# Kernel optimization log

Hardware: AMD Instinct MI355X
Metric: run time of the kernel (lower is better)

The kernel has to match this reference:

```python
import jax, jax.numpy as jnp
import numpy as np

INPUT_DIM, HIDDEN_DIM, OUTPUT_DIM = 64, 256, 32
BATCH, SEQ = 256, 1024
# AutoNCP(256, 32, sparsity_level=0.5): motor=32, command=max(int(0.4*224),1)=89, inter=135
LAYER_HID = [135, 89, 32]
LAYER_IN = [INPUT_DIM, 135, 89]


def setup_inputs() -> dict:
    key = jax.random.key(0)
    ks = iter(jax.random.split(key, 64))
    d = {}
    d["x"] = jax.random.normal(next(ks), (BATCH, SEQ, INPUT_DIM), dtype=jnp.float32)
    for l, (fin, hid) in enumerate(zip(LAYER_IN, LAYER_HID)):
        sp = jax.random.bernoulli(next(ks), 0.5, (hid, fin))
        d[f"mask{l}"] = jnp.concatenate([sp, jnp.ones((hid, hid), dtype=bool)], axis=1)
        scale = 1.0 / np.sqrt(fin + hid)
        for name in ("W1", "W2", "Wa", "Wb"):
            d[f"{name}_{l}"] = jax.random.normal(next(ks), (hid, fin + hid), dtype=jnp.float32) * scale
        for name in ("b1", "b2", "ba", "bb"):
            d[f"{name}_{l}"] = jnp.zeros((hid,), dtype=jnp.float32)
    d["fc_W"] = jax.random.normal(next(ks), (HIDDEN_DIM, HIDDEN_DIM), dtype=jnp.float32) * (1.0 / np.sqrt(HIDDEN_DIM))
    d["fc_b"] = jnp.zeros((HIDDEN_DIM,), dtype=jnp.float32)
    return d


def _cfc_cell(inp, h, mask, W1, b1, W2, b2, Wa, ba, Wb, bb):
    # ncps CfCCell, mode='default', no backbone, ts = 1.0
    x = jnp.concatenate([inp, h], axis=1)
    m = mask.astype(W1.dtype)
    ff1 = jnp.tanh(x @ (W1 * m).T + b1)
    ff2 = jnp.tanh(x @ (W2 * m).T + b2)
    t = jax.nn.sigmoid(x @ Wa.T + ba + x @ Wb.T + bb)  # sigmoid(t_a*ts + t_b), ts=1
    return ff1 * (1.0 - t) + t * ff2


def _forward(x, masks, layer_params, fc_W, fc_b):
    B = x.shape[0]
    init = tuple(jnp.zeros((B, h), dtype=x.dtype) for h in LAYER_HID)

    def step(carry, xt):
        hs = list(carry)
        inp = xt
        for l in range(3):  # inter -> command -> motor (WiredCfCCell)
            hs[l] = _cfc_cell(inp, hs[l], masks[l], *layer_params[l])
            inp = hs[l]
        return tuple(hs), None

    carry, _ = jax.lax.scan(step, init, jnp.swapaxes(x, 0, 1))  # scan over time [T,B,D]
    hn = jnp.concatenate(carry, axis=1)  # [B, HIDDEN_DIM] full state
    return hn @ fc_W.T + fc_b


def reference(x, mask0, mask1, mask2,
              W1_0, b1_0, W2_0, b2_0, Wa_0, ba_0, Wb_0, bb_0,
              W1_1, b1_1, W2_1, b2_1, Wa_1, ba_1, Wb_1, bb_1,
              W1_2, b1_2, W2_2, b2_2, Wa_2, ba_2, Wb_2, bb_2,
              fc_W, fc_b):
    masks = (mask0, mask1, mask2)
    lp = ((W1_0, b1_0, W2_0, b2_0, Wa_0, ba_0, Wb_0, bb_0),
          (W1_1, b1_1, W2_1, b2_1, Wa_1, ba_1, Wb_1, bb_1),
          (W1_2, b1_2, W2_2, b2_2, Wa_2, ba_2, Wb_2, bb_2))
    return _forward(x, masks, lp, fc_W, fc_b)
```

## Files before the change

### kernel.cpp

```cpp
#include <hip/hip_runtime.h>


typedef _Float16 half2v __attribute__((ext_vector_type(2)));
typedef _Float16 half8v __attribute__((ext_vector_type(8)));

#define NBLK   256
#define NTHR   512
#define TSTEPS 1024
#define KPAD   224
#define WSTRIDE 232
#define KHALF  112
#define NKB    14

struct Ptrs {
    const float* x;
    const unsigned int* msk[3];
    const float* W1[3];
    const float* W2[3];
    const float* Wa[3];
    const float* Wb[3];
    const float* b1[3];
    const float* b2[3];
    const float* ba[3];
    const float* bb[3];
    const float* fcW;
    const float* fcb;
};

__device__ __forceinline__ float fexp2(float x) {
#if __has_builtin(__builtin_amdgcn_exp2f)
    return __builtin_amdgcn_exp2f(x);
#else
    return exp2f(x);
#endif
}
__device__ __forceinline__ float frcp(float x) {
#if __has_builtin(__builtin_amdgcn_rcpf)
    return __builtin_amdgcn_rcpf(x);
#else
    return 1.0f / x;
#endif
}
__device__ __forceinline__ float fsig(float x) {
    return frcp(1.0f + fexp2(-1.442695041f * x));
}
__device__ __forceinline__ float ftanh(float x) {
    return 2.0f * frcp(1.0f + fexp2(-2.885390082f * x)) - 1.0f;
}

#if __has_builtin(__builtin_amdgcn_fdot2)
#define FD(a, b, c) __builtin_amdgcn_fdot2((a), (b), (c), false)
#else
__device__ __forceinline__ float fd_fallback(half2v a, half2v b, float c) {
    return c + (float)a[0] * (float)b[0] + (float)a[1] * (float)b[1];
}
#define FD(a, b, c) fd_fallback((a), (b), (c))
#endif

__device__ __forceinline__ half2v h2(_Float16 a, _Float16 b) { return half2v{a, b}; }

__device__ __forceinline__ half2v fold2(const float* Wp, const unsigned int* mkp,
                                        int nK, int K, int k0) {
    float u0 = 0.f, u1 = 0.f;
    if (k0 < K) {
        const int i0 = nK + k0;
        u0 = Wp[i0] * ((mkp[i0] != 0u) ? 1.0f : 0.0f);
    }
    if (k0 + 1 < K) {
        const int i1 = nK + k0 + 1;
        u1 = Wp[i1] * ((mkp[i1] != 0u) ? 1.0f : 0.0f);
    }
    return h2((_Float16)u0, (_Float16)u1);
}

#define DECL_KB(kb) \
    const half2v w1_##kb##_0 = fold2(W1p, mkp, nK, K, koff + kb * 8 + 0); \
    const half2v w1_##kb##_1 = fold2(W1p, mkp, nK, K, koff + kb * 8 + 2); \
    const half2v w1_##kb##_2 = fold2(W1p, mkp, nK, K, koff + kb * 8 + 4); \
    const half2v w1_##kb##_3 = fold2(W1p, mkp, nK, K, koff + kb * 8 + 6); \
    const half2v w2_##kb##_0 = fold2(W2p, mkp, nK, K, koff + kb * 8 + 0); \
    const half2v w2_##kb##_1 = fold2(W2p, mkp, nK, K, koff + kb * 8 + 2); \
    const half2v w2_##kb##_2 = fold2(W2p, mkp, nK, K, koff + kb * 8 + 4); \
    const half2v w2_##kb##_3 = fold2(W2p, mkp, nK, K, koff + kb * 8 + 6);

#define DOT_KB(kb) { \
    const half8v xv = *(const half8v*)(srcp + kb * 8); \
    const half8v wv = *(const half8v*)(wap + kb * 8); \
    ac00 = FD(h2(xv[0], xv[1]), w1_##kb##_0, ac00); \
    ac10 = FD(h2(xv[0], xv[1]), w2_##kb##_0, ac10); \
    ac20 = FD(h2(xv[0], xv[1]), h2(wv[0], wv[1]), ac20); \
    ac01 = FD(h2(xv[2], xv[3]), w1_##kb##_1, ac01); \
    ac11 = FD(h2(xv[2], xv[3]), w2_##kb##_1, ac11); \
    ac21 = FD(h2(xv[2], xv[3]), h2(wv[2], wv[3]), ac21); \
    ac00 = FD(h2(xv[4], xv[5]), w1_##kb##_2, ac00); \
    ac10 = FD(h2(xv[4], xv[5]), w2_##kb##_2, ac10); \
    ac20 = FD(h2(xv[4], xv[5]), h2(wv[4], wv[5]), ac20); \
    ac01 = FD(h2(xv[6], xv[7]), w1_##kb##_3, ac01); \
    ac11 = FD(h2(xv[6], xv[7]), w2_##kb##_3, ac11); \
    ac21 = FD(h2(xv[6], xv[7]), h2(wv[6], wv[7]), ac21); \
}

__global__ __launch_bounds__(NTHR, 2)
void cfc_kernel(Ptrs P, float* __restrict__ out) {
    __shared__ __align__(16) _Float16 xc[2][3][KPAD];
    __shared__ __align__(16) _Float16 waL[256][WSTRIDE];
    __shared__ __align__(16) float hn[256];

    const int tid  = threadIdx.x;
    const int b    = blockIdx.x;
    const int unit = tid >> 1;
    const int half = tid & 1;

    int L, n;
    if (unit < 135)      { L = 0; n = unit; }
    else if (unit < 224) { L = 1; n = unit - 135; }
    else                 { L = 2; n = unit - 224; }
    const int K    = (L == 0) ? 199 : ((L == 1) ? 224 : 121);
    const int HOFF = (L == 0) ? 0   : ((L == 1) ? 135 : 224);

    {
        int* z = (int*)&xc[0][0][0];
        for (int i = tid; i < 2 * 3 * KPAD / 2; i += NTHR) z[i] = 0;
    }

    const float* W1p        = P.W1[L];
    const float* W2p        = P.W2[L];
    const float* Wap        = P.Wa[L];
    const float* Wbp        = P.Wb[L];
    const unsigned int* mkp = P.msk[L];
    const int nK   = n * K;
    const int koff = half * KHALF;

    DECL_KB(0)  DECL_KB(1)  DECL_KB(2)  DECL_KB(3)  DECL_KB(4)
    DECL_KB(5)  DECL_KB(6)  DECL_KB(7)  DECL_KB(8)  DECL_KB(9)
    DECL_KB(10) DECL_KB(11) DECL_KB(12) DECL_KB(13)

#pragma unroll
    for (int i = 0; i < KHALF / 2; ++i) {
        const int k0 = koff + 2 * i;
        float a0 = 0.f, a1 = 0.f;
        if (k0 < K)     a0 = Wap[nK + k0] + Wbp[nK + k0];
        if (k0 + 1 < K) a1 = Wap[nK + k0 + 1] + Wbp[nK + k0 + 1];
        *(half2v*)&waL[unit][k0] = h2((_Float16)a0, (_Float16)a1);
    }

    const float bv1 = P.b1[L][n];
    const float bv2 = P.b2[L][n];
    const float bva = P.ba[L][n] + P.bb[L][n];

    const int xlane = tid - (NTHR - 64);
    float xpend = 0.0f;
    if (xlane >= 0) {
        xc[0][0][xlane] = (_Float16)P.x[((size_t)b * TSTEPS + 0) * 64 + xlane];
        xpend           = P.x[((size_t)b * TSTEPS + 1) * 64 + xlane];
    }
    __syncthreads();

    const _Float16* wap = &waL[unit][koff];
    const _Float16* s0p = &xc[0][L][koff];
    const _Float16* s1p = &xc[1][L][koff];

    for (int tick = 0; tick < TSTEPS + 2; ++tick) {
        if (xlane >= 0) {
            if (tick + 1 < TSTEPS)
                xc[(tick + 1) & 1][0][xlane] = (_Float16)xpend;
            if (tick + 2 < TSTEPS)
                xpend = P.x[((size_t)b * TSTEPS + (tick + 2)) * 64 + xlane];
        }

        const int s = tick - L;
        if (s >= 0 && s < TSTEPS) {
            const _Float16* srcp = (s & 1) ? s1p : s0p;
            float ac00 = 0.f, ac01 = 0.f, ac10 = 0.f, ac11 = 0.f, ac20 = 0.f, ac21 = 0.f;
            DOT_KB(0)  DOT_KB(1)  DOT_KB(2)  DOT_KB(3)  DOT_KB(4)
            DOT_KB(5)  DOT_KB(6)  DOT_KB(7)  DOT_KB(8)  DOT_KB(9)
            DOT_KB(10) DOT_KB(11) DOT_KB(12) DOT_KB(13)

            float s1 = ac00 + ac01;
            float s2 = ac10 + ac11;
            float sa = ac20 + ac21;
            s1 += __shfl_xor(s1, 1, 64);
            s2 += __shfl_xor(s2, 1, 64);
            sa += __shfl_xor(sa, 1, 64);
            const float f1 = ftanh(s1 + bv1);
            const float f2 = ftanh(s2 + bv2);
            const float tg = fsig(sa + bva);
            const float h  = f1 + tg * (f2 - f1);
            const _Float16 hv = (_Float16)h;

            const int pA = s & 1;
            const int pB = (s + 1) & 1;
            if (half == 0) {
                if (L == 0)      xc[pA][1][n] = hv;
                else if (L == 1) xc[pA][2][n] = hv;
                if (s == TSTEPS - 1) hn[HOFF + n] = h;
            } else {
                if (L == 0)      xc[pB][0][64 + n]  = hv;
                else if (L == 1) xc[pB][1][135 + n] = hv;
                else             xc[pB][2][89 + n]  = hv;
            }
        }
        __syncthreads();
    }

    {
        const int o = unit;
        const float4* wr = (const float4*)(P.fcW + (size_t)o * 256 + half * 128);
        const float4* hr = (const float4*)(hn + half * 128);
        float acc = half ? 0.0f : P.fcb[o];
#pragma unroll 8
        for (int d = 0; d < 32; ++d) {
            const float4 a = hr[d];
            const float4 w = wr[d];
            acc += a.x * w.x + a.y * w.y + a.z * w.z + a.w * w.w;
        }
        acc += __shfl_xor(acc, 1, 64);
        if (half == 0) out[(size_t)b * 256 + o] = acc;
    }
}

extern "C" void kernel_launch(void* const* d_in, const int* in_sizes, int n_in,
                              void* d_out, int out_size, void* d_ws, size_t ws_size,
                              hipStream_t stream) {
    (void)in_sizes; (void)n_in; (void)out_size; (void)d_ws; (void)ws_size;
    Ptrs P;
    P.x = (const float*)d_in[0];
    for (int l = 0; l < 3; ++l) {
        const int base = 1 + l * 9;
        P.msk[l] = (const unsigned int*)d_in[base + 0];
        P.W1[l]  = (const float*)d_in[base + 1];
        P.W2[l]  = (const float*)d_in[base + 2];
        P.Wa[l]  = (const float*)d_in[base + 3];
        P.Wb[l]  = (const float*)d_in[base + 4];
        P.b1[l]  = (const float*)d_in[base + 5];
        P.b2[l]  = (const float*)d_in[base + 6];
        P.ba[l]  = (const float*)d_in[base + 7];
        P.bb[l]  = (const float*)d_in[base + 8];
    }
    P.fcW = (const float*)d_in[28];
    P.fcb = (const float*)d_in[29];

    hipLaunchKernelGGL(cfc_kernel, dim3(NBLK), dim3(NTHR), 0, stream,
                       P, (float*)d_out);
}
```

Before: 1.649 ms.

## Keep all gate weights in registers and share x loads via DPP

```diff
diff --git a/kernel.cpp b/kernel.cpp
--- a/kernel.cpp
+++ b/kernel.cpp
@@ -3,14 +3,13 @@
 
 typedef _Float16 half2v __attribute__((ext_vector_type(2)));
 typedef _Float16 half8v __attribute__((ext_vector_type(8)));
+typedef int      int4v  __attribute__((ext_vector_type(4)));
 
 #define NBLK   256
 #define NTHR   512
 #define TSTEPS 1024
 #define KPAD   224
-#define WSTRIDE 232
 #define KHALF  112
-#define NKB    14
 
 struct Ptrs {
     const float* x;
@@ -59,6 +58,21 @@
 
 __device__ __forceinline__ half2v h2(_Float16 a, _Float16 b) { return half2v{a, b}; }
 
+__device__ __forceinline__ half8v dpp_xor2(half8v v) {
+    int4v a = __builtin_bit_cast(int4v, v);
+    int4v r;
+    r[0] = __builtin_amdgcn_update_dpp(0, a[0], 0x4E, 0xF, 0xF, true);
+    r[1] = __builtin_amdgcn_update_dpp(0, a[1], 0x4E, 0xF, 0xF, true);
+    r[2] = __builtin_amdgcn_update_dpp(0, a[2], 0x4E, 0xF, 0xF, true);
+    r[3] = __builtin_amdgcn_update_dpp(0, a[3], 0x4E, 0xF, 0xF, true);
+    return __builtin_bit_cast(half8v, r);
+}
+__device__ __forceinline__ float pair_sum(float x) {
+    const int v = __builtin_amdgcn_update_dpp(
+        0, __builtin_bit_cast(int, x), 0xB1, 0xF, 0xF, true);
+    return x + __builtin_bit_cast(float, v);
+}
+
 __device__ __forceinline__ half2v fold2(const float* Wp, const unsigned int* mkp,
                                         int nK, int K, int k0) {
     float u0 = 0.f, u1 = 0.f;
@@ -73,43 +87,38 @@
     return h2((_Float16)u0, (_Float16)u1);
 }
 
-#define DECL_KB(kb) \
-    const half2v w1_##kb##_0 = fold2(W1p, mkp, nK, K, koff + kb * 8 + 0); \
-    const half2v w1_##kb##_1 = fold2(W1p, mkp, nK, K, koff + kb * 8 + 2); \
-    const half2v w1_##kb##_2 = fold2(W1p, mkp, nK, K, koff + kb * 8 + 4); \
-    const half2v w1_##kb##_3 = fold2(W1p, mkp, nK, K, koff + kb * 8 + 6); \
-    const half2v w2_##kb##_0 = fold2(W2p, mkp, nK, K, koff + kb * 8 + 0); \
-    const half2v w2_##kb##_1 = fold2(W2p, mkp, nK, K, koff + kb * 8 + 2); \
-    const half2v w2_##kb##_2 = fold2(W2p, mkp, nK, K, koff + kb * 8 + 4); \
-    const half2v w2_##kb##_3 = fold2(W2p, mkp, nK, K, koff + kb * 8 + 6);
-
-#define DOT_KB(kb) { \
-    const half8v xv = *(const half8v*)(srcp + kb * 8); \
-    const half8v wv = *(const half8v*)(wap + kb * 8); \
-    ac00 = FD(h2(xv[0], xv[1]), w1_##kb##_0, ac00); \
-    ac10 = FD(h2(xv[0], xv[1]), w2_##kb##_0, ac10); \
-    ac20 = FD(h2(xv[0], xv[1]), h2(wv[0], wv[1]), ac20); \
-    ac01 = FD(h2(xv[2], xv[3]), w1_##kb##_1, ac01); \
-    ac11 = FD(h2(xv[2], xv[3]), w2_##kb##_1, ac11); \
-    ac21 = FD(h2(xv[2], xv[3]), h2(wv[2], wv[3]), ac21); \
-    ac00 = FD(h2(xv[4], xv[5]), w1_##kb##_2, ac00); \
-    ac10 = FD(h2(xv[4], xv[5]), w2_##kb##_2, ac10); \
-    ac20 = FD(h2(xv[4], xv[5]), h2(wv[4], wv[5]), ac20); \
-    ac01 = FD(h2(xv[6], xv[7]), w1_##kb##_3, ac01); \
-    ac11 = FD(h2(xv[6], xv[7]), w2_##kb##_3, ac11); \
-    ac21 = FD(h2(xv[6], xv[7]), h2(wv[6], wv[7]), ac21); \
-}
-
-__global__ __launch_bounds__(NTHR, 2)
+#define DOTS(m, xo_, xt_) { \
+    const half2v o0 = h2(xo_[0], xo_[1]), o1 = h2(xo_[2], xo_[3]); \
+    const half2v o2 = h2(xo_[4], xo_[5]), o3 = h2(xo_[6], xo_[7]); \
+    const half2v t0 = h2(xt_[0], xt_[1]), t1 = h2(xt_[2], xt_[3]); \
+    const half2v t2 = h2(xt_[4], xt_[5]), t3 = h2(xt_[6], xt_[7]); \
+    ac00 = FD(o0, w1o[4*(m)+0], ac00);  ac01 = FD(t0, w1t[4*(m)+0], ac01); \
+    ac10 = FD(o0, w2o[4*(m)+0], ac10);  ac11 = FD(t0, w2t[4*(m)+0], ac11); \
+    ac20 = FD(o0, wao[4*(m)+0], ac20);  ac21 = FD(t0, wat[4*(m)+0], ac21); \
+    ac00 = FD(o1, w1o[4*(m)+1], ac00);  ac01 = FD(t1, w1t[4*(m)+1], ac01); \
+    ac10 = FD(o1, w2o[4*(m)+1], ac10);  ac11 = FD(t1, w2t[4*(m)+1], ac11); \
+    ac20 = FD(o1, wao[4*(m)+1], ac20);  ac21 = FD(t1, wat[4*(m)+1], ac21); \
+    ac00 = FD(o2, w1o[4*(m)+2], ac00);  ac01 = FD(t2, w1t[4*(m)+2], ac01); \
+    ac10 = FD(o2, w2o[4*(m)+2], ac10);  ac11 = FD(t2, w2t[4*(m)+2], ac11); \
+    ac20 = FD(o2, wao[4*(m)+2], ac20);  ac21 = FD(t2, wat[4*(m)+2], ac21); \
+    ac00 = FD(o3, w1o[4*(m)+3], ac00);  ac01 = FD(t3, w1t[4*(m)+3], ac01); \
+    ac10 = FD(o3, w2o[4*(m)+3], ac10);  ac11 = FD(t3, w2t[4*(m)+3], ac11); \
+    ac20 = FD(o3, wao[4*(m)+3], ac20);  ac21 = FD(t3, wat[4*(m)+3], ac21); \
+}
+
+__global__ __launch_bounds__(NTHR)
+__attribute__((amdgpu_waves_per_eu(2, 2)))
 void cfc_kernel(Ptrs P, float* __restrict__ out) {
     __shared__ __align__(16) _Float16 xc[2][3][KPAD];
-    __shared__ __align__(16) _Float16 waL[256][WSTRIDE];
     __shared__ __align__(16) float hn[256];
 
     const int tid  = threadIdx.x;
     const int b    = blockIdx.x;
     const int unit = tid >> 1;
     const int half = tid & 1;
+    const int up   = unit & 1;
+
+    const bool direct = ((tid >> 6) == 4);
 
     int L, n;
     if (unit < 135)      { L = 0; n = unit; }
@@ -121,6 +130,14 @@
     {
         int* z = (int*)&xc[0][0][0];
         for (int i = tid; i < 2 * 3 * KPAD / 2; i += NTHR) z[i] = 0;
+    }
+    __syncthreads();
+
+    const int xlane = tid - 448;
+    float xpend = 0.0f;
+    if (xlane >= 0) {
+        xc[0][0][xlane] = (_Float16)P.x[((size_t)b * TSTEPS + 0) * 64 + xlane];
+        xpend           = P.x[((size_t)b * TSTEPS + 1) * 64 + xlane];
     }
 
     const float* W1p        = P.W1[L];
@@ -131,34 +148,35 @@
     const int nK   = n * K;
     const int koff = half * KHALF;
 
-    DECL_KB(0)  DECL_KB(1)  DECL_KB(2)  DECL_KB(3)  DECL_KB(4)
-    DECL_KB(5)  DECL_KB(6)  DECL_KB(7)  DECL_KB(8)  DECL_KB(9)
-    DECL_KB(10) DECL_KB(11) DECL_KB(12) DECL_KB(13)
-
-#pragma unroll
-    for (int i = 0; i < KHALF / 2; ++i) {
-        const int k0 = koff + 2 * i;
-        float a0 = 0.f, a1 = 0.f;
-        if (k0 < K)     a0 = Wap[nK + k0] + Wbp[nK + k0];
-        if (k0 + 1 < K) a1 = Wap[nK + k0 + 1] + Wbp[nK + k0 + 1];
-        *(half2v*)&waL[unit][k0] = h2((_Float16)a0, (_Float16)a1);
-    }
-
+    half2v w1o[28], w1t[28], w2o[28], w2t[28], wao[28], wat[28];
+#pragma unroll
+    for (int m = 0; m < 7; ++m) {
+#pragma unroll
+        for (int j = 0; j < 4; ++j) {
+            const int ko = koff + (2 * m + up) * 8 + 2 * j;
+            const int kt = koff + (2 * m + 1 - up) * 8 + 2 * j;
+            w1o[m * 4 + j] = fold2(W1p, mkp, nK, K, ko);
+            w1t[m * 4 + j] = fold2(W1p, mkp, nK, K, kt);
+            w2o[m * 4 + j] = fold2(W2p, mkp, nK, K, ko);
+            w2t[m * 4 + j] = fold2(W2p, mkp, nK, K, kt);
+            {
+                float a0 = 0.f, a1 = 0.f;
+                if (ko < K)     a0 = Wap[nK + ko] + Wbp[nK + ko];
+                if (ko + 1 < K) a1 = Wap[nK + ko + 1] + Wbp[nK + ko + 1];
+                wao[m * 4 + j] = h2((_Float16)a0, (_Float16)a1);
+            }
+            {
+                float a0 = 0.f, a1 = 0.f;
+                if (kt < K)     a0 = Wap[nK + kt] + Wbp[nK + kt];
+                if (kt + 1 < K) a1 = Wap[nK + kt + 1] + Wbp[nK + kt + 1];
+                wat[m * 4 + j] = h2((_Float16)a0, (_Float16)a1);
+            }
+        }
+    }
     const float bv1 = P.b1[L][n];
     const float bv2 = P.b2[L][n];
     const float bva = P.ba[L][n] + P.bb[L][n];
-
-    const int xlane = tid - (NTHR - 64);
-    float xpend = 0.0f;
-    if (xlane >= 0) {
-        xc[0][0][xlane] = (_Float16)P.x[((size_t)b * TSTEPS + 0) * 64 + xlane];
-        xpend           = P.x[((size_t)b * TSTEPS + 1) * 64 + xlane];
-    }
     __syncthreads();
-
-    const _Float16* wap = &waL[unit][koff];
-    const _Float16* s0p = &xc[0][L][koff];
-    const _Float16* s1p = &xc[1][L][koff];
 
     for (int tick = 0; tick < TSTEPS + 2; ++tick) {
         if (xlane >= 0) {
@@ -170,18 +188,29 @@
 
         const int s = tick - L;
         if (s >= 0 && s < TSTEPS) {
-            const _Float16* srcp = (s & 1) ? s1p : s0p;
+            const _Float16* srcp = &xc[s & 1][L][koff];
+            const _Float16* po   = srcp + up * 8;
+            const _Float16* pt   = srcp + (1 - up) * 8;
             float ac00 = 0.f, ac01 = 0.f, ac10 = 0.f, ac11 = 0.f, ac20 = 0.f, ac21 = 0.f;
-            DOT_KB(0)  DOT_KB(1)  DOT_KB(2)  DOT_KB(3)  DOT_KB(4)
-            DOT_KB(5)  DOT_KB(6)  DOT_KB(7)  DOT_KB(8)  DOT_KB(9)
-            DOT_KB(10) DOT_KB(11) DOT_KB(12) DOT_KB(13)
-
-            float s1 = ac00 + ac01;
-            float s2 = ac10 + ac11;
-            float sa = ac20 + ac21;
-            s1 += __shfl_xor(s1, 1, 64);
-            s2 += __shfl_xor(s2, 1, 64);
-            sa += __shfl_xor(sa, 1, 64);
+            if (!direct) {
+#pragma unroll
+                for (int m = 0; m < 7; ++m) {
+                    const half8v xown = *(const half8v*)(po + m * 16);
+                    const half8v xoth = dpp_xor2(xown);
+                    DOTS(m, xown, xoth);
+                }
+            } else {
+#pragma unroll
+                for (int m = 0; m < 7; ++m) {
+                    const half8v xown = *(const half8v*)(po + m * 16);
+                    const half8v xoth = *(const half8v*)(pt + m * 16);
+                    DOTS(m, xown, xoth);
+                }
+            }
+
+            const float s1 = pair_sum(ac00 + ac01);
+            const float s2 = pair_sum(ac10 + ac11);
+            const float sa = pair_sum(ac20 + ac21);
             const float f1 = ftanh(s1 + bv1);
             const float f2 = ftanh(s2 + bv2);
             const float tg = fsig(sa + bva);
@@ -214,7 +243,7 @@
             const float4 w = wr[d];
             acc += a.x * w.x + a.y * w.y + a.z * w.z + a.w * w.w;
         }
-        acc += __shfl_xor(acc, 1, 64);
+        acc = pair_sum(acc);
         if (half == 0) out[(size_t)b * 256 + o] = acc;
     }
 }
```

New measurement: 1.564 ms. -5.2%, faster.
